# Optimization experiments

Measured on AMD Instinct MI355X. Metric: run time of the kernel, lower is better.

Reference implementation:

```python
import jax, jax.numpy as jnp
import numpy as np

EPS = 1e-6
NUM_HEADS = 16

def _rms(x, w=None):
    y = x * jax.lax.rsqrt(jnp.mean(x * x, axis=-1, keepdims=True) + EPS)
    return y if w is None else y * w

def _rope(q, k, pos):
    # q,k: [B,H,T,Dh]; half-split (rotate_half) RoPE convention, base 10000
    dh = q.shape[-1]
    half = dh // 2
    freqs = 1.0 / (10000.0 ** (jnp.arange(half, dtype=jnp.float32) / half))
    ang = pos.astype(jnp.float32)[:, None] * freqs[None, :]  # [T, half]
    cos = jnp.concatenate([jnp.cos(ang), jnp.cos(ang)], -1)  # [T, Dh]
    sin = jnp.concatenate([jnp.sin(ang), jnp.sin(ang)], -1)
    def rot(v):
        v1, v2 = jnp.split(v, 2, axis=-1)
        return jnp.concatenate([-v2, v1], -1)
    return q * cos + rot(q) * sin, k * cos + rot(k) * sin


def setup_inputs() -> dict:
    key = jax.random.key(0)
    ks = jax.random.split(key, 12)
    B, T, D, H = 2, 2048, 1024, NUM_HEADS
    Dh = D // H
    Hm = 2816  # SwiGLU hidden: multiple_of*ceil(int(2*4*D/3)/256)
    s = lambda fan_in: 1.0 / np.sqrt(fan_in)
    return {
        "x": jax.random.normal(ks[0], (B, T, D), jnp.float32),
        "c": jax.random.normal(ks[1], (B, D), jnp.float32),
        "pos": jnp.arange(T, dtype=jnp.int32),
        "adaln_w": jax.random.normal(ks[2], (D, 6 * D), jnp.float32) * s(D) * 0.1,
        "adaln_b": jax.random.normal(ks[3], (6 * D,), jnp.float32) * 0.02,
        "qkv_w": jax.random.normal(ks[4], (D, 3 * D), jnp.float32) * s(D),
        "lnq_w": jnp.ones((Dh,), jnp.float32),
        "lnk_w": jnp.ones((Dh,), jnp.float32),
        "proj_w": jax.random.normal(ks[5], (D, D), jnp.float32) * s(D),
        "proj_b": jnp.zeros((D,), jnp.float32),
        "w1_w": jax.random.normal(ks[6], (D, Hm), jnp.float32) * s(D),
        "w3_w": jax.random.normal(ks[7], (D, Hm), jnp.float32) * s(D),
        "w2_w": jax.random.normal(ks[8], (Hm, D), jnp.float32) * s(Hm),
    }


def reference(x, c, pos, adaln_w, adaln_b, qkv_w, lnq_w, lnk_w, proj_w, proj_b, w1_w, w3_w, w2_w):
    B, T, D = x.shape
    H = NUM_HEADS
    Dh = D // H

    # AdaLN: SiLU -> Linear -> chunk(6)
    mods = jax.nn.silu(c) @ adaln_w + adaln_b  # [B,6D]
    shift_msa, scale_msa, gate_msa, shift_mlp, scale_mlp, gate_mlp = jnp.split(mods, 6, axis=-1)

    # norm1 (RMSNorm, no affine) + modulate along seq dim
    x_mod = _rms(x) * (1.0 + scale_msa[:, None, :]) + shift_msa[:, None, :]

    # QKV projection (no bias)
    qkv = x_mod @ qkv_w  # [B,T,3D]
    q, k, v = jnp.split(qkv, 3, axis=-1)
    q = q.reshape(B, T, H, Dh).transpose(0, 2, 1, 3)  # [B,H,T,Dh]
    k = k.reshape(B, T, H, Dh).transpose(0, 2, 1, 3)
    v = v.reshape(B, T, H, Dh).transpose(0, 2, 1, 3)

    # per-head RMS qk-norm with affine weight
    q = _rms(q, lnq_w)
    k = _rms(k, lnk_w)

    # 1D RoPE
    q, k = _rope(q, k, pos)

    # attention core (SDPA, delegated in the original module)
    scores = jnp.einsum('bhqd,bhkd->bhqk', q, k) / jnp.sqrt(jnp.float32(Dh))
    attn = jax.nn.softmax(scores, axis=-1)
    attn_out = jnp.einsum('bhqk,bhkd->bhqd', attn, v)  # [B,H,T,Dh]
    attn_out = attn_out.transpose(0, 2, 1, 3).reshape(B, T, D)

    # post_attention: gated residual + SwiGLU MLP
    x = x + gate_msa[:, None, :] * (attn_out @ proj_w + proj_b)
    h = _rms(x) * (1.0 + scale_mlp[:, None, :]) + shift_mlp[:, None, :]
    mlp = (jax.nn.silu(h @ w1_w) * (h @ w3_w)) @ w2_w
    x = x + gate_mlp[:, None, :] * mlp
    return x
```

## Files before the change

kernel.cpp:

```cpp
#include <hip/hip_runtime.h>
#include <stdint.h>
#include <math.h>

typedef unsigned short u16;
typedef __attribute__((ext_vector_type(4))) float f32x4;
typedef __attribute__((ext_vector_type(16))) float f32x16;
typedef __attribute__((ext_vector_type(8))) __bf16 bf16x8;

#define DEV static __device__ __forceinline__

typedef __attribute__((address_space(1))) void gvoid;
typedef __attribute__((address_space(3))) void lvoid;

DEV float bf2f(u16 u){ uint32_t v = ((uint32_t)u) << 16; float f; __builtin_memcpy(&f, &v, 4); return f; }
DEV u16 f2bf(float f){ uint32_t v; __builtin_memcpy(&v, &f, 4); v = (v + 0x7fffu + ((v >> 16) & 1u)) >> 16; return (u16)v; }

DEV void cp16(const void* g, void* l){
  __builtin_amdgcn_global_load_lds((gvoid*)g, (lvoid*)l, 16, 0, 0);
}
DEV f32x4 mfma16(bf16x8 a, bf16x8 b, f32x4 c){
  return __builtin_amdgcn_mfma_f32_16x16x32_bf16(a, b, c, 0, 0, 0);
}
DEV f32x16 mfma32(bf16x8 a, bf16x8 b, f32x16 c){
  return __builtin_amdgcn_mfma_f32_32x32x16_bf16(a, b, c, 0, 0, 0);
}
DEV uint32_t cvtpk(float a, float b){
  uint32_t r;
  asm volatile("v_cvt_pk_bf16_f32 %0, %1, %2" : "=v"(r) : "v"(a), "v"(b));
  return r;
}
DEV void uswap(uint32_t& a, uint32_t& b){
  asm volatile("v_permlane32_swap_b32 %0, %1" : "+v"(a), "+v"(b));
}
DEV void fswap(float& a, float& b){
  asm volatile("v_permlane32_swap_b32 %0, %1" : "+v"(a), "+v"(b));
}
DEV float fexp2(float x){
  float r;
  asm("v_exp_f32 %0, %1" : "=v"(r) : "v"(x));
  return r;
}

DEV void slab_remap(int SX, int SY, int& bx, int& by)
{
  const int GX = gridDim.x;
  const int h = blockIdx.y * GX + blockIdx.x;
  const int x = h & 7, s = h >> 3;
  const int ssz = SX * SY;
  const int nsx = GX / SX;
  const int slab = x + 8 * (s / ssz);
  const int ws = s % ssz;
  bx = (slab % nsx) * SX + ws % SX;
  by = (slab / nsx) * SY + ws / SX;
}

DEV int swz32(int r){ return (r & 3) ^ ((r >> 2) & 3); }

__global__ void __launch_bounds__(256) adaln1(const float* __restrict__ c,
                                              const float* __restrict__ w,
                                              float* __restrict__ part)
{
  __shared__ float sc[256];
  int k0 = blockIdx.y * 128;
  {
    int i = threadIdx.x;
    int b = i >> 7, kk = i & 127;
    float v = c[b * 1024 + k0 + kk];
    sc[i] = v / (1.f + __expf(-v));
  }
  __syncthreads();
  int col = blockIdx.x * 256 + threadIdx.x;
  float a0 = 0.f, a1 = 0.f;
  #pragma unroll 8
  for (int k = 0; k < 128; ++k){
    float wv = w[(size_t)(k0 + k) * 6144 + col];
    a0 += sc[k] * wv;
    a1 += sc[128 + k] * wv;
  }
  part[((size_t)blockIdx.y * 2 + 0) * 6144 + col] = a0;
  part[((size_t)blockIdx.y * 2 + 1) * 6144 + col] = a1;
}

__global__ void __launch_bounds__(256) adaln2(const float* __restrict__ part,
                                              const float* __restrict__ bias,
                                              float* __restrict__ mods)
{
  int i = blockIdx.x * 256 + threadIdx.x;
  int b = i / 6144, col = i % 6144;
  float a = bias[col];
  #pragma unroll
  for (int r = 0; r < 8; ++r) a += part[((size_t)r * 2 + b) * 6144 + col];
  mods[i] = a;
}

__global__ void __launch_bounds__(256) rope_table(const int* __restrict__ pos,
                                                  float* __restrict__ ct,
                                                  float* __restrict__ st)
{
  int idx = blockIdx.x * 256 + threadIdx.x;
  int t = idx >> 5, i = idx & 31;
  float freq = expf(-0.28782313662425575f * (float)i);
  float ang = (float)pos[t] * freq;
  ct[idx] = cosf(ang);
  st[idx] = sinf(ang);
}

__global__ void __launch_bounds__(256) rmsmod(const float* __restrict__ x,
                                              const float* __restrict__ mods,
                                              u16* __restrict__ out,
                                              int shift_off, int scale_off)
{
  __shared__ float wsum[4];
  int row = blockIdx.x;
  int b = row >> 11;
  const float4 v = ((const float4*)(x + (size_t)row * 1024))[threadIdx.x];
  float ss = v.x * v.x + v.y * v.y + v.z * v.z + v.w * v.w;
  #pragma unroll
  for (int m = 1; m < 64; m <<= 1) ss += __shfl_xor(ss, m);
  if ((threadIdx.x & 63) == 0) wsum[threadIdx.x >> 6] = ss;
  __syncthreads();
  float tot = wsum[0] + wsum[1] + wsum[2] + wsum[3];
  float rr = rsqrtf(tot * (1.f / 1024.f) + 1e-6f);
  const float* mb = mods + (size_t)b * 6144;
  int d0 = threadIdx.x * 4;
  ushort4 o;
  o.x = f2bf(v.x * rr * (1.f + mb[scale_off + d0 + 0]) + mb[shift_off + d0 + 0]);
  o.y = f2bf(v.y * rr * (1.f + mb[scale_off + d0 + 1]) + mb[shift_off + d0 + 1]);
  o.z = f2bf(v.z * rr * (1.f + mb[scale_off + d0 + 2]) + mb[shift_off + d0 + 2]);
  o.w = f2bf(v.w * rr * (1.f + mb[scale_off + d0 + 3]) + mb[shift_off + d0 + 3]);
  ((ushort4*)(out + (size_t)row * 1024))[threadIdx.x] = o;
}

__global__ void __launch_bounds__(256) transpose_w(const float* __restrict__ in,
                                                   u16* __restrict__ out, int R, int C)
{
  __shared__ float t[32][33];
  int tx = threadIdx.x & 31, ty = threadIdx.x >> 5;
  int c0 = blockIdx.x * 32, r0 = blockIdx.y * 32;
  #pragma unroll
  for (int i = 0; i < 4; ++i) t[ty + 8 * i][tx] = in[(size_t)(r0 + ty + 8 * i) * C + c0 + tx];
  __syncthreads();
  #pragma unroll
  for (int i = 0; i < 4; ++i) out[(size_t)(c0 + ty + 8 * i) * R + r0 + tx] = f2bf(t[tx][ty + 8 * i]);
}

__global__ void __launch_bounds__(256) vtrans(const u16* __restrict__ qkv,
                                              u16* __restrict__ vt)
{
  __shared__ u16 tile[32][33];
  int tx = threadIdx.x & 31, ty = threadIdx.x >> 5;
  int t0 = blockIdx.x * 32;
  int d0 = blockIdx.y * 32;
  int bh = blockIdx.z; int b = bh >> 4, h = bh & 15;
  #pragma unroll
  for (int i = 0; i < 4; ++i) {
    int t = t0 + ty + 8 * i;
    tile[ty + 8 * i][tx] = qkv[((size_t)(b * 2048 + t)) * 3072 + 2048 + h * 64 + d0 + tx];
  }
  __syncthreads();
  #pragma unroll
  for (int i = 0; i < 4; ++i) {
    int d = d0 + ty + 8 * i;
    vt[((size_t)bh * 64 + d) * 2048 + t0 + tx] = tile[tx][ty + 8 * i];
  }
}

__global__ void __launch_bounds__(256) gemm_bt(const u16* __restrict__ A,
                                               const u16* __restrict__ Bt,
                                               int M, int N, int K,
                                               int SX, int SY,
                                               u16* __restrict__ outb)
{
  __shared__ __align__(16) u16 Ash[128 * 32];
  __shared__ __align__(16) u16 Bsh[128 * 32];
  const int tid = threadIdx.x;
  const int l = tid & 63, w = tid >> 6;
  int bx, by; slab_remap(SX, SY, bx, by);
  const int m0 = by * 128, n0 = bx * 128;
  const int wr = (w >> 1) * 64, wc = (w & 1) * 64;
  const int fr = l & 15, fg = l >> 4;
  f32x4 acc[4][4] = {};

  for (int kt = 0; kt < K; kt += 32) {
    __syncthreads();
    #pragma unroll
    for (int p = 0; p < 2; ++p) {
      int slot = p * 256 + tid;
      int r = slot >> 2, kp = slot & 3;
      int kpg = kp ^ swz32(r);
      cp16(A + (size_t)(m0 + r) * K + kt + kpg * 8, Ash + slot * 8);
      cp16(Bt + (size_t)(n0 + r) * K + kt + kpg * 8, Bsh + slot * 8);
    }
    __syncthreads();
    bf16x8 af[4], bfr[4];
    #pragma unroll
    for (int m = 0; m < 4; ++m) {
      int r = wr + m * 16 + fr;
      af[m] = *(const bf16x8*)(Ash + r * 32 + ((fg ^ swz32(r)) << 3));
    }
    #pragma unroll
    for (int n = 0; n < 4; ++n) {
      int r = wc + n * 16 + fr;
      bfr[n] = *(const bf16x8*)(Bsh + r * 32 + ((fg ^ swz32(r)) << 3));
    }
    #pragma unroll
    for (int m = 0; m < 4; ++m)
      #pragma unroll
      for (int n = 0; n < 4; ++n)
        acc[m][n] = mfma16(af[m], bfr[n], acc[m][n]);
  }

  #pragma unroll
  for (int m = 0; m < 4; ++m)
  #pragma unroll
  for (int n = 0; n < 4; ++n)
  #pragma unroll
  for (int j = 0; j < 4; ++j) {
    int row = m0 + wr + m * 16 + fg * 4 + j;
    int col = n0 + wc + n * 16 + fr;
    outb[(size_t)row * N + col] = f2bf(acc[m][n][j]);
  }
}

template<int EPI>
__global__ void __launch_bounds__(256) gemm_skinny(const u16* __restrict__ A,
                                                   const u16* __restrict__ Bt,
                                                   int M, int N, int K,
                                                   const float* __restrict__ mods,
                                                   int gate_off,
                                                   const float* __restrict__ bias,
                                                   const float* __restrict__ res,
                                                   float* __restrict__ outf)
{
  __shared__ __align__(16) u16 Ash[2][64 * 64];
  __shared__ __align__(16) u16 Bsh[2][128 * 64];
  const int tid = threadIdx.x;
  const int l = tid & 63, w = tid >> 6;
  int bx, by; slab_remap(2, 16, bx, by);
  const int m0 = by * 64, n0 = bx * 128;
  const int wr = (w >> 1) * 32, wc = (w & 1) * 64;
  const int fr = l & 15, fg = l >> 4;
  const int sw = fr & 7;
  const int nk = K >> 6;
  f32x4 acc[2][4] = {};

  auto stage = [&](int kt, int bsel) {
    #pragma unroll
    for (int p = 0; p < 2; ++p) {
      int slot = p * 256 + tid;
      int r = slot >> 3, kp = slot & 7;
      int kpg = kp ^ (r & 7);
      cp16(A + (size_t)(m0 + r) * K + kt + kpg * 8, &Ash[bsel][slot * 8]);
    }
    #pragma unroll
    for (int p = 0; p < 4; ++p) {
      int slot = p * 256 + tid;
      int r = slot >> 3, kp = slot & 7;
      int kpg = kp ^ (r & 7);
      cp16(Bt + (size_t)(n0 + r) * K + kt + kpg * 8, &Bsh[bsel][slot * 8]);
    }
  };

  stage(0, 0);
  __syncthreads();

  for (int t = 0; t < nk; ++t) {
    if (t + 1 < nk) stage((t + 1) << 6, (t + 1) & 1);
    const u16* Ab = Ash[t & 1];
    const u16* Bb = Bsh[t & 1];
    #pragma unroll
    for (int kk = 0; kk < 2; ++kk) {
      const int coff = ((kk * 4 + fg) ^ sw) * 8;
      bf16x8 af[2], bfr[4];
      #pragma unroll
      for (int m = 0; m < 2; ++m) af[m] = *(const bf16x8*)(Ab + (wr + m * 16 + fr) * 64 + coff);
      #pragma unroll
      for (int n = 0; n < 4; ++n) bfr[n] = *(const bf16x8*)(Bb + (wc + n * 16 + fr) * 64 + coff);
      #pragma unroll
      for (int m = 0; m < 2; ++m)
        #pragma unroll
        for (int n = 0; n < 4; ++n)
          acc[m][n] = mfma16(af[m], bfr[n], acc[m][n]);
    }
    __syncthreads();
  }

  #pragma unroll
  for (int m = 0; m < 2; ++m)
  #pragma unroll
  for (int n = 0; n < 4; ++n)
  #pragma unroll
  for (int j = 0; j < 4; ++j) {
    int row = m0 + wr + m * 16 + fg * 4 + j;
    int col = n0 + wc + n * 16 + fr;
    size_t idx = (size_t)row * N + col;
    float v = acc[m][n][j];
    int b = row >> 11;
    if (EPI == 1)
      outf[idx] = res[idx] + mods[(size_t)b * 6144 + gate_off + col] * (v + bias[col]);
    else
      outf[idx] = res[idx] + mods[(size_t)b * 6144 + gate_off + col] * v;
  }
}

__global__ void __launch_bounds__(256) gemm_w13(const u16* __restrict__ A,
                                                const u16* __restrict__ B1t,
                                                const u16* __restrict__ B3t,
                                                u16* __restrict__ outb)
{
  const int K = 1024, N = 2816;
  __shared__ __align__(16) u16 Ash[128 * 32];
  __shared__ __align__(16) u16 B1sh[64 * 32];
  __shared__ __align__(16) u16 B3sh[64 * 32];
  const int tid = threadIdx.x;
  const int l = tid & 63, w = tid >> 6;
  int bx, by; slab_remap(11, 4, bx, by);
  const int m0 = by * 128, n0 = bx * 64;
  const int wr = (w >> 1) * 64, wc = (w & 1) * 32;
  const int fr = l & 15, fg = l >> 4;
  f32x4 acc1[4][2] = {}, acc3[4][2] = {};

  for (int kt = 0; kt < K; kt += 32) {
    __syncthreads();
    #pragma unroll
    for (int p = 0; p < 2; ++p) {
      int slot = p * 256 + tid;
      int r = slot >> 2, kp = slot & 3;
      int kpg = kp ^ swz32(r);
      cp16(A + (size_t)(m0 + r) * K + kt + kpg * 8, Ash + slot * 8);
    }
    {
      int slot = tid;
      int r = slot >> 2, kp = slot & 3;
      int kpg = kp ^ swz32(r);
      cp16(B1t + (size_t)(n0 + r) * K + kt + kpg * 8, B1sh + slot * 8);
      cp16(B3t + (size_t)(n0 + r) * K + kt + kpg * 8, B3sh + slot * 8);
    }
    __syncthreads();
    bf16x8 af[4], b1f[2], b3f[2];
    #pragma unroll
    for (int m = 0; m < 4; ++m) {
      int r = wr + m * 16 + fr;
      af[m] = *(const bf16x8*)(Ash + r * 32 + ((fg ^ swz32(r)) << 3));
    }
    #pragma unroll
    for (int n = 0; n < 2; ++n) {
      int r = wc + n * 16 + fr;
      b1f[n] = *(const bf16x8*)(B1sh + r * 32 + ((fg ^ swz32(r)) << 3));
      b3f[n] = *(const bf16x8*)(B3sh + r * 32 + ((fg ^ swz32(r)) << 3));
    }
    #pragma unroll
    for (int m = 0; m < 4; ++m)
      #pragma unroll
      for (int n = 0; n < 2; ++n) {
        acc1[m][n] = mfma16(af[m], b1f[n], acc1[m][n]);
        acc3[m][n] = mfma16(af[m], b3f[n], acc3[m][n]);
      }
  }

  #pragma unroll
  for (int m = 0; m < 4; ++m)
  #pragma unroll
  for (int n = 0; n < 2; ++n)
  #pragma unroll
  for (int j = 0; j < 4; ++j) {
    int row = m0 + wr + m * 16 + fg * 4 + j;
    int col = n0 + wc + n * 16 + fr;
    float v1 = acc1[m][n][j];
    float v3 = acc3[m][n][j];
    float s = v1 / (1.f + __expf(-v1));
    outb[(size_t)row * N + col] = f2bf(s * v3);
  }
}

__global__ void __launch_bounds__(256) qknorm_rope(const u16* __restrict__ qkv,
                                                   const float* __restrict__ lnq,
                                                   const float* __restrict__ lnk,
                                                   const float* __restrict__ ctab,
                                                   const float* __restrict__ stab,
                                                   u16* __restrict__ qo,
                                                   u16* __restrict__ ko)
{
  int r = blockIdx.x * 4 + (threadIdx.x >> 6);
  int l = threadIdx.x & 63;
  int h = r & 15, t = (r >> 4) & 2047, b = r >> 15;
  const u16* base = qkv + ((size_t)(b * 2048 + t)) * 3072 + h * 64 + l;
  float q = bf2f(base[0]);
  float k = bf2f(base[1024]);
  float sq = q * q, sk = k * k;
  #pragma unroll
  for (int m = 1; m < 64; m <<= 1) { sq += __shfl_xor(sq, m); sk += __shfl_xor(sk, m); }
  float rq = rsqrtf(sq * (1.f / 64.f) + 1e-6f);
  float rk = rsqrtf(sk * (1.f / 64.f) + 1e-6f);
  float yq = q * rq * lnq[l];
  float yk = k * rk * lnk[l];
  float cs = ctab[t * 32 + (l & 31)];
  float sn = stab[t * 32 + (l & 31)];
  float pq = __shfl_xor(yq, 32);
  float pk = __shfl_xor(yk, 32);
  float rotq = (l < 32) ? -pq : pq;
  float rotk = (l < 32) ? -pk : pk;
  float oq = (yq * cs + rotq * sn) * 0.1803368801111204f;
  float ok = yk * cs + rotk * sn;
  size_t oidx = ((size_t)(b * 16 + h) * 2048 + t) * 64 + l;
  qo[oidx] = f2bf(oq);
  ko[oidx] = f2bf(ok);
}

__global__ void __launch_bounds__(256, 2) flash_attn(const u16* __restrict__ qg,
                                                     const u16* __restrict__ kg,
                                                     const u16* __restrict__ vtg,
                                                     u16* __restrict__ og)
{
  __shared__ __align__(16) char smem[65536];
  const int tid = threadIdx.x, l = tid & 63, w = tid >> 6;
  const int lq = l & 31, hi = l >> 5;
  const int swz = lq & 7;
  const int xcd = blockIdx.x & 7, slot = blockIdx.x >> 3;
  const int g = slot >> 4, qt = slot & 15;
  const int bh = g * 8 + xcd;
  const int h = bh & 15, b = bh >> 4;

  bf16x8 qf[4];
  {
    const u16* qp = qg + ((size_t)bh * 2048 + qt * 128 + w * 32 + lq) * 64 + hi * 8;
    #pragma unroll
    for (int ks = 0; ks < 4; ++ks) qf[ks] = *(const bf16x8*)(qp + ks * 16);
  }
  const u16* kgb = kg + (size_t)bh * 2048 * 64;
  const u16* vgb = vtg + (size_t)bh * 64 * 2048;

  auto stage = [&](int kv, int bsel) {
    #pragma unroll
    for (int p = 0; p < 4; ++p) {
      int s2 = p * 256 + tid;
      int r = s2 >> 3, cl = s2 & 7;
      int cg = cl ^ (r & 7);
      cp16(kgb + (size_t)(kv + r) * 64 + cg * 8, smem + bsel * 16384 + s2 * 16);
    }
    #pragma unroll
    for (int p = 0; p < 4; ++p) {
      int s2 = p * 256 + tid;
      int r = s2 >> 4, cl = s2 & 15;
      int cg = cl ^ (r & 7);
      cp16(vgb + (size_t)r * 2048 + kv + cg * 8, smem + 32768 + bsel * 16384 + s2 * 16);
    }
  };

  f32x16 ob0 = {}, ob1 = {};
  float l_run = 0.f;

  stage(0, 0);
  __syncthreads();

  for (int t = 0; t < 16; ++t) {
    const int cur = t & 1;
    stage(((t + 1) & 15) * 128, cur ^ 1);
    const char* Kb = smem + cur * 16384;
    const char* Vb = smem + 32768 + cur * 16384;

    #pragma unroll
    for (int ko = 0; ko < 128; ko += 64) {
      f32x16 s0 = {}, s1 = {};
      __builtin_amdgcn_s_setprio(1);
      #pragma unroll
      for (int ks = 0; ks < 4; ++ks) {
        const int c = hi + ks * 2;
        bf16x8 kf0 = *(const bf16x8*)(Kb + (ko + lq) * 128 + ((c ^ swz) << 4));
        bf16x8 kf1 = *(const bf16x8*)(Kb + (ko + 32 + lq) * 128 + ((c ^ swz) << 4));
        s0 = mfma32(kf0, qf[ks], s0);
        s1 = mfma32(kf1, qf[ks], s1);
      }
      __builtin_amdgcn_s_setprio(0);
      #pragma unroll
      for (int r = 0; r < 16; ++r) s0[r] = fexp2(s0[r]);
      #pragma unroll
      for (int r = 0; r < 16; ++r) s1[r] = fexp2(s1[r]);
      {
        float t0 = (s0[0] + s0[1]) + (s0[2] + s0[3]);
        float t1 = (s0[4] + s0[5]) + (s0[6] + s0[7]);
        float t2 = (s0[8] + s0[9]) + (s0[10] + s0[11]);
        float t3 = (s0[12] + s0[13]) + (s0[14] + s0[15]);
        float u0 = (s1[0] + s1[1]) + (s1[2] + s1[3]);
        float u1 = (s1[4] + s1[5]) + (s1[6] + s1[7]);
        float u2 = (s1[8] + s1[9]) + (s1[10] + s1[11]);
        float u3 = (s1[12] + s1[13]) + (s1[14] + s1[15]);
        float ls = ((t0 + t1) + (t2 + t3)) + ((u0 + u1) + (u2 + u3));
        float lo = ls;
        fswap(ls, lo);
        l_run += ls + lo;
      }
      uint32_t pw[16];
      {
        uint32_t x0 = cvtpk(s0[0], s0[1]),   y0 = cvtpk(s0[4], s0[5]);   uswap(x0, y0);
        uint32_t x1 = cvtpk(s0[2], s0[3]),   y1 = cvtpk(s0[6], s0[7]);   uswap(x1, y1);
        uint32_t x2 = cvtpk(s0[8], s0[9]),   y2 = cvtpk(s0[12], s0[13]); uswap(x2, y2);
        uint32_t x3 = cvtpk(s0[10], s0[11]), y3 = cvtpk(s0[14], s0[15]); uswap(x3, y3);
        pw[0] = x0; pw[1] = x1; pw[2] = y0; pw[3] = y1;
        pw[4] = x2; pw[5] = x3; pw[6] = y2; pw[7] = y3;
      }
      {
        uint32_t x0 = cvtpk(s1[0], s1[1]),   y0 = cvtpk(s1[4], s1[5]);   uswap(x0, y0);
        uint32_t x1 = cvtpk(s1[2], s1[3]),   y1 = cvtpk(s1[6], s1[7]);   uswap(x1, y1);
        uint32_t x2 = cvtpk(s1[8], s1[9]),   y2 = cvtpk(s1[12], s1[13]); uswap(x2, y2);
        uint32_t x3 = cvtpk(s1[10], s1[11]), y3 = cvtpk(s1[14], s1[15]); uswap(x3, y3);
        pw[8] = x0;  pw[9] = x1;  pw[10] = y0; pw[11] = y1;
        pw[12] = x2; pw[13] = x3; pw[14] = y2; pw[15] = y3;
      }
      __builtin_amdgcn_s_setprio(1);
      #pragma unroll
      for (int ks = 0; ks < 4; ++ks) {
        union { uint32_t u[4]; bf16x8 v; } pk_;
        pk_.u[0] = pw[ks * 4 + 0]; pk_.u[1] = pw[ks * 4 + 1];
        pk_.u[2] = pw[ks * 4 + 2]; pk_.u[3] = pw[ks * 4 + 3];
        const int c = (ko >> 3) + ks * 2 + hi;
        bf16x8 vf0 = *(const bf16x8*)(Vb + lq * 256 + ((c ^ swz) << 4));
        bf16x8 vf1 = *(const bf16x8*)(Vb + (32 + lq) * 256 + ((c ^ swz) << 4));
        ob0 = mfma32(vf0, pk_.v, ob0);
        ob1 = mfma32(vf1, pk_.v, ob1);
      }
      __builtin_amdgcn_s_setprio(0);
    }
    __syncthreads();
  }

  float invl = 1.0f / l_run;
  char* ob_base = smem + w * 4096 + lq * 128 + 8 * hi;
  #pragma unroll
  for (int g2 = 0; g2 < 4; ++g2) {
    uint2 t2;
    t2.x = cvtpk(ob0[g2 * 4 + 0] * invl, ob0[g2 * 4 + 1] * invl);
    t2.y = cvtpk(ob0[g2 * 4 + 2] * invl, ob0[g2 * 4 + 3] * invl);
    *(uint2*)(ob_base + ((g2 ^ (lq & 7)) << 4)) = t2;
    uint2 t3;
    t3.x = cvtpk(ob1[g2 * 4 + 0] * invl, ob1[g2 * 4 + 1] * invl);
    t3.y = cvtpk(ob1[g2 * 4 + 2] * invl, ob1[g2 * 4 + 3] * invl);
    *(uint2*)(ob_base + (((g2 + 4) ^ (lq & 7)) << 4)) = t3;
  }
  __syncthreads();
  #pragma unroll
  for (int i = 0; i < 4; ++i) {
    int idx = i * 256 + tid;
    int ww = idx >> 8, q = (idx >> 3) & 31, s = idx & 7;
    uint4 val = *(const uint4*)(smem + ww * 4096 + q * 128 + ((s ^ (q & 7)) << 4));
    int t = qt * 128 + ww * 32 + q;
    *(uint4*)(og + ((size_t)(b * 2048 + t)) * 1024 + h * 64 + s * 8) = val;
  }
}

extern "C" void kernel_launch(void* const* d_in, const int* in_sizes, int n_in,
                              void* d_out, int out_size, void* d_ws, size_t ws_size,
                              hipStream_t stream)
{
  (void)in_sizes; (void)n_in; (void)out_size; (void)ws_size;
  const float* x       = (const float*)d_in[0];
  const float* c       = (const float*)d_in[1];
  const int*   pos     = (const int*)d_in[2];
  const float* adaln_w = (const float*)d_in[3];
  const float* adaln_b = (const float*)d_in[4];
  const float* qkv_w   = (const float*)d_in[5];
  const float* lnq     = (const float*)d_in[6];
  const float* lnk     = (const float*)d_in[7];
  const float* proj_w  = (const float*)d_in[8];
  const float* proj_b  = (const float*)d_in[9];
  const float* w1_w    = (const float*)d_in[10];
  const float* w3_w    = (const float*)d_in[11];
  const float* w2_w    = (const float*)d_in[12];
  float* out = (float*)d_out;

  char* ws = (char*)d_ws;
  size_t off = 0;
  auto alloc = [&](size_t bytes) -> char* {
    char* p = ws + off; off += (bytes + 255) & ~(size_t)255; return p;
  };
  float* part    = (float*)alloc((size_t)8 * 2 * 6144 * 4);
  float* mods    = (float*)alloc((size_t)2 * 6144 * 4);
  float* ctab    = (float*)alloc((size_t)2048 * 32 * 4);
  float* stab    = (float*)alloc((size_t)2048 * 32 * 4);
  u16* qkv_wt    = (u16*)alloc((size_t)3072 * 1024 * 2);
  u16* proj_wt   = (u16*)alloc((size_t)1024 * 1024 * 2);
  u16* w1_wt     = (u16*)alloc((size_t)2816 * 1024 * 2);
  u16* w3_wt     = (u16*)alloc((size_t)2816 * 1024 * 2);
  u16* w2_wt     = (u16*)alloc((size_t)1024 * 2816 * 2);
  float* x1      = (float*)alloc((size_t)4096 * 1024 * 4);
  u16* attn_bf   = (u16*)alloc((size_t)4096 * 1024 * 2);
  char* pool = ws + off;
  u16* xmod_bf   = (u16*)(pool);
  u16* qkv_bf    = (u16*)(pool + 8388608);
  u16* q_bf      = (u16*)(pool + 33554432);
  u16* k_bf      = (u16*)(pool + 41943040);
  u16* vt_bf     = (u16*)(pool + 50331648);
  u16* h_bf      = (u16*)(pool);
  u16* hidden_bf = (u16*)(pool + 31457280);

  adaln1<<<dim3(24, 8), 256, 0, stream>>>(c, adaln_w, part);
  adaln2<<<48, 256, 0, stream>>>(part, adaln_b, mods);
  rope_table<<<256, 256, 0, stream>>>(pos, ctab, stab);
  rmsmod<<<4096, 256, 0, stream>>>(x, mods, xmod_bf, 0, 1024);
  transpose_w<<<dim3(96, 32), 256, 0, stream>>>(qkv_w, qkv_wt, 1024, 3072);
  transpose_w<<<dim3(32, 32), 256, 0, stream>>>(proj_w, proj_wt, 1024, 1024);
  transpose_w<<<dim3(88, 32), 256, 0, stream>>>(w1_w, w1_wt, 1024, 2816);
  transpose_w<<<dim3(88, 32), 256, 0, stream>>>(w3_w, w3_wt, 1024, 2816);
  transpose_w<<<dim3(32, 88), 256, 0, stream>>>(w2_w, w2_wt, 2816, 1024);

  gemm_bt<<<dim3(24, 32), 256, 0, stream>>>(xmod_bf, qkv_wt, 4096, 3072, 1024, 6, 8, qkv_bf);
  qknorm_rope<<<16384, 256, 0, stream>>>(qkv_bf, lnq, lnk, ctab, stab, q_bf, k_bf);
  vtrans<<<dim3(64, 2, 32), 256, 0, stream>>>(qkv_bf, vt_bf);
  flash_attn<<<512, 256, 0, stream>>>(q_bf, k_bf, vt_bf, attn_bf);
  gemm_skinny<1><<<dim3(8, 64), 256, 0, stream>>>(attn_bf, proj_wt, 4096, 1024, 1024,
                                                  mods, 2048, proj_b, x, x1);
  rmsmod<<<4096, 256, 0, stream>>>(x1, mods, h_bf, 3072, 4096);
  gemm_w13<<<dim3(44, 32), 256, 0, stream>>>(h_bf, w1_wt, w3_wt, hidden_bf);
  gemm_skinny<4><<<dim3(8, 64), 256, 0, stream>>>(hidden_bf, w2_wt, 4096, 1024, 2816,
                                                  mods, 5120, nullptr, x1, out);
}
```

Baseline: 257.6 us.

## Double-buffer LDS tiles in QKV and W1/W3 GEMMs to overlap loads with MFMA

Converts the gemm_bt and gemm_w13 main loops to use two LDS buffers. The next K-slice is issued with global_load_lds while MFMAs consume the current buffer, and the per-iteration barrier pair drops to a single barrier at the end. This aims to hide global-to-LDS latency behind compute. It doubles LDS use per block, which may reduce occupancy, and its correctness depends on the asynchronous LDS loads completing before the trailing barrier.

```diff
diff --git a/kernel.cpp b/kernel.cpp
--- a/kernel.cpp
+++ b/kernel.cpp
@@ -171,43 +171,52 @@
                                                int SX, int SY,
                                                u16* __restrict__ outb)
 {
-  __shared__ __align__(16) u16 Ash[128 * 32];
-  __shared__ __align__(16) u16 Bsh[128 * 32];
+  __shared__ __align__(16) u16 Ash[2][128 * 32];
+  __shared__ __align__(16) u16 Bsh[2][128 * 32];
   const int tid = threadIdx.x;
   const int l = tid & 63, w = tid >> 6;
   int bx, by; slab_remap(SX, SY, bx, by);
   const int m0 = by * 128, n0 = bx * 128;
   const int wr = (w >> 1) * 64, wc = (w & 1) * 64;
   const int fr = l & 15, fg = l >> 4;
+  const int nk = K >> 5;
   f32x4 acc[4][4] = {};
 
-  for (int kt = 0; kt < K; kt += 32) {
-    __syncthreads();
+  auto stage = [&](int kt, int bsel) {
     #pragma unroll
     for (int p = 0; p < 2; ++p) {
       int slot = p * 256 + tid;
       int r = slot >> 2, kp = slot & 3;
       int kpg = kp ^ swz32(r);
-      cp16(A + (size_t)(m0 + r) * K + kt + kpg * 8, Ash + slot * 8);
-      cp16(Bt + (size_t)(n0 + r) * K + kt + kpg * 8, Bsh + slot * 8);
-    }
-    __syncthreads();
+      cp16(A + (size_t)(m0 + r) * K + kt + kpg * 8, &Ash[bsel][slot * 8]);
+      cp16(Bt + (size_t)(n0 + r) * K + kt + kpg * 8, &Bsh[bsel][slot * 8]);
+    }
+  };
+
+  stage(0, 0);
+  __syncthreads();
+
+  for (int t = 0; t < nk; ++t) {
+    if (t + 1 < nk) stage((t + 1) << 5, (t + 1) & 1);
+    const u16* Ab = Ash[t & 1];
+    const u16* Bb = Bsh[t & 1];
     bf16x8 af[4], bfr[4];
     #pragma unroll
     for (int m = 0; m < 4; ++m) {
       int r = wr + m * 16 + fr;
-      af[m] = *(const bf16x8*)(Ash + r * 32 + ((fg ^ swz32(r)) << 3));
+      af[m] = *(const bf16x8*)(Ab + r * 32 + ((fg ^ swz32(r)) << 3));
     }
     #pragma unroll
     for (int n = 0; n < 4; ++n) {
       int r = wc + n * 16 + fr;
-      bfr[n] = *(const bf16x8*)(Bsh + r * 32 + ((fg ^ swz32(r)) << 3));
+      bfr[n] = *(const bf16x8*)(Bb + r * 32 + ((fg ^ swz32(r)) << 3));
     }
     #pragma unroll
     for (int m = 0; m < 4; ++m)
       #pragma unroll
       for (int n = 0; n < 4; ++n)
         acc[m][n] = mfma16(af[m], bfr[n], acc[m][n]);
+    __syncthreads();
   }
 
   #pragma unroll
@@ -309,9 +318,9 @@
                                                 u16* __restrict__ outb)
 {
   const int K = 1024, N = 2816;
-  __shared__ __align__(16) u16 Ash[128 * 32];
-  __shared__ __align__(16) u16 B1sh[64 * 32];
-  __shared__ __align__(16) u16 B3sh[64 * 32];
+  __shared__ __align__(16) u16 Ash[2][128 * 32];
+  __shared__ __align__(16) u16 B1sh[2][64 * 32];
+  __shared__ __align__(16) u16 B3sh[2][64 * 32];
   const int tid = threadIdx.x;
   const int l = tid & 63, w = tid >> 6;
   int bx, by; slab_remap(11, 4, bx, by);
@@ -320,34 +329,42 @@
   const int fr = l & 15, fg = l >> 4;
   f32x4 acc1[4][2] = {}, acc3[4][2] = {};
 
-  for (int kt = 0; kt < K; kt += 32) {
-    __syncthreads();
+  auto stage = [&](int kt, int bsel) {
     #pragma unroll
     for (int p = 0; p < 2; ++p) {
       int slot = p * 256 + tid;
       int r = slot >> 2, kp = slot & 3;
       int kpg = kp ^ swz32(r);
-      cp16(A + (size_t)(m0 + r) * K + kt + kpg * 8, Ash + slot * 8);
+      cp16(A + (size_t)(m0 + r) * K + kt + kpg * 8, &Ash[bsel][slot * 8]);
     }
     {
       int slot = tid;
       int r = slot >> 2, kp = slot & 3;
       int kpg = kp ^ swz32(r);
-      cp16(B1t + (size_t)(n0 + r) * K + kt + kpg * 8, B1sh + slot * 8);
-      cp16(B3t + (size_t)(n0 + r) * K + kt + kpg * 8, B3sh + slot * 8);
-    }
-    __syncthreads();
+      cp16(B1t + (size_t)(n0 + r) * K + kt + kpg * 8, &B1sh[bsel][slot * 8]);
+      cp16(B3t + (size_t)(n0 + r) * K + kt + kpg * 8, &B3sh[bsel][slot * 8]);
+    }
+  };
+
+  stage(0, 0);
+  __syncthreads();
+
+  for (int t = 0; t < 32; ++t) {
+    if (t + 1 < 32) stage((t + 1) << 5, (t + 1) & 1);
+    const u16* Ab  = Ash[t & 1];
+    const u16* B1b = B1sh[t & 1];
+    const u16* B3b = B3sh[t & 1];
     bf16x8 af[4], b1f[2], b3f[2];
     #pragma unroll
     for (int m = 0; m < 4; ++m) {
       int r = wr + m * 16 + fr;
-      af[m] = *(const bf16x8*)(Ash + r * 32 + ((fg ^ swz32(r)) << 3));
+      af[m] = *(const bf16x8*)(Ab + r * 32 + ((fg ^ swz32(r)) << 3));
     }
     #pragma unroll
     for (int n = 0; n < 2; ++n) {
       int r = wc + n * 16 + fr;
-      b1f[n] = *(const bf16x8*)(B1sh + r * 32 + ((fg ^ swz32(r)) << 3));
-      b3f[n] = *(const bf16x8*)(B3sh + r * 32 + ((fg ^ swz32(r)) << 3));
+      b1f[n] = *(const bf16x8*)(B1b + r * 32 + ((fg ^ swz32(r)) << 3));
+      b3f[n] = *(const bf16x8*)(B3b + r * 32 + ((fg ^ swz32(r)) << 3));
     }
     #pragma unroll
     for (int m = 0; m < 4; ++m)
@@ -356,6 +373,7 @@
         acc1[m][n] = mfma16(af[m], b1f[n], acc1[m][n]);
         acc3[m][n] = mfma16(af[m], b3f[n], acc3[m][n]);
       }
+    __syncthreads();
   }
 
   #pragma unroll
```

New measurement: 267.5 us. 3.8% more time.
